# Kernel optimization log

Measured on AMD Instinct MI355X. Metric: run time of the kernel, lower is better.

Reference implementation:

```python
import jax, jax.numpy as jnp
import numpy as np

K = 1024  # attention hidden dim
H = 1024  # encoder hidden dim


def setup_inputs() -> dict:
    key = jax.random.key(0)
    ks = jax.random.split(key, 8)
    B, S = 32, 2048
    decoder_state = jax.random.normal(ks[0], (B, H), dtype=jnp.float32)
    encoder_hiddens = jax.random.normal(ks[1], (B, S, H), dtype=jnp.float32)
    # Linear params (torch convention: y = x @ W.T + b)
    Wa_w = jax.random.normal(ks[2], (1, K), dtype=jnp.float32) / np.sqrt(K)
    Wa_b = jnp.zeros((1,), dtype=jnp.float32)
    Wb_w = jax.random.normal(ks[3], (K, H), dtype=jnp.float32) / np.sqrt(H)
    Wb_b = jnp.zeros((K,), dtype=jnp.float32)
    Wc_w = jax.random.normal(ks[4], (K, H), dtype=jnp.float32) / np.sqrt(H)
    Wc_b = jnp.zeros((K,), dtype=jnp.float32)
    return {
        "decoder_state": decoder_state,
        "encoder_hiddens": encoder_hiddens,
        "Wa_w": Wa_w, "Wa_b": Wa_b,
        "Wb_w": Wb_w, "Wb_b": Wb_b,
        "Wc_w": Wc_w, "Wc_b": Wc_b,
    }


def reference(decoder_state, encoder_hiddens, Wa_w, Wa_b, Wb_w, Wb_b, Wc_w, Wc_b):
    # dec_proj: [B, K]; enc_proj: [B, S, K]
    dec_proj = decoder_state @ Wb_w.T + Wb_b
    enc_proj = jnp.einsum('bsh,kh->bsk', encoder_hiddens, Wc_w) + Wc_b
    # additive score: tanh then project to scalar -> [B, S]
    e = jnp.tanh(dec_proj[:, None, :] + enc_proj)
    scores = jnp.einsum('bsk,k->bs', e, Wa_w[0]) + Wa_b[0]
    attn = jax.nn.softmax(scores, axis=1)
    # weighted sum over sequence -> [B, H]
    context = jnp.einsum('bs,bsh->bh', attn, encoder_hiddens)
    return context
```

## Files before the change

kernel.cpp:

```cpp
#include <hip/hip_runtime.h>
#include <hip/hip_bf16.h>
#include <stdint.h>

#define B_SZ 32
#define S_SZ 2048
#define H_SZ 1024
#define K_SZ 1024
#define M_SZ (B_SZ * S_SZ)

typedef __attribute__((ext_vector_type(8))) short bf16x8;
typedef __attribute__((ext_vector_type(4))) float f32x4;


__device__ __forceinline__ short f2bf_rne(float f) {
    uint32_t u = __builtin_bit_cast(uint32_t, f);
    u += 0x7fffu + ((u >> 16) & 1u);
    return (short)(u >> 16);
}

__device__ __forceinline__ float fast_tanh(float x) {
    float ex = __expf(2.0f * x);
    return 1.0f - 2.0f / (ex + 1.0f);
}


__global__ void cvt_bf16_k(const float* __restrict__ in,
                           __hip_bfloat16* __restrict__ out, int n8) {
    int idx = blockIdx.x * blockDim.x + threadIdx.x;
    int stride = gridDim.x * blockDim.x;
    for (int i = idx; i < n8; i += stride) {
        const float4* p = (const float4*)in + (size_t)i * 2;
        float4 a = p[0], b = p[1];
        bf16x8 r;
        r[0] = f2bf_rne(a.x); r[1] = f2bf_rne(a.y);
        r[2] = f2bf_rne(a.z); r[3] = f2bf_rne(a.w);
        r[4] = f2bf_rne(b.x); r[5] = f2bf_rne(b.y);
        r[6] = f2bf_rne(b.z); r[7] = f2bf_rne(b.w);
        ((bf16x8*)out)[i] = r;
    }
}


__global__ __launch_bounds__(256) void decproj_k(
    const float* __restrict__ ds, const float* __restrict__ Wb,
    const float* __restrict__ Wb_b, const float* __restrict__ Wc_b,
    float* __restrict__ dp) {
    int g = blockIdx.x * 4 + (threadIdx.x >> 6);
    int lane = threadIdx.x & 63;
    int b = g >> 10;
    int k = g & 1023;
    const float4* wrow = (const float4*)(Wb + (size_t)k * H_SZ);
    const float4* xrow = (const float4*)(ds + (size_t)b * H_SZ);
    float sum = 0.f;
#pragma unroll
    for (int it = 0; it < 4; it++) {
        float4 w = wrow[lane + it * 64];
        float4 x = xrow[lane + it * 64];
        sum += w.x * x.x + w.y * x.y + w.z * x.z + w.w * x.w;
    }
#pragma unroll
    for (int off = 1; off < 64; off <<= 1) sum += __shfl_xor(sum, off, 64);
    if (lane == 0) dp[g] = sum + Wb_b[k] + Wc_b[k];
}


template <bool AF32>
__global__ __launch_bounds__(256) void gemm_scores_k(
    const void* __restrict__ Aptr, const __hip_bfloat16* __restrict__ Bw,
    const float* __restrict__ decp, const float* __restrict__ Wa,
    float* __restrict__ sp) {
    constexpr int ABYTES = AF32 ? 128 * 32 * 4 : 128 * 32 * 2;
    __shared__ __align__(16) unsigned char AsmRaw[ABYTES];
    __shared__ __align__(16) unsigned char BsmRaw[128 * 32 * 2];

    const int t = threadIdx.x;
    const int wave = t >> 6;
    const int lane = t & 63;
    const int wm = wave >> 1, wn = wave & 1;
    const int quad = lane >> 4;
    const int l15 = lane & 15;

    const int colBlk = blockIdx.x & 7;
    const int rowBlk = blockIdx.x >> 3;
    const int row0 = rowBlk * 128;
    const int col0 = colBlk * 128;
    const int b = row0 >> 11;

    f32x4 acc[4][4];
#pragma unroll
    for (int i = 0; i < 4; i++)
#pragma unroll
        for (int j = 0; j < 4; j++) acc[i][j] = f32x4{0.f, 0.f, 0.f, 0.f};

    const __hip_bfloat16* Ab = (const __hip_bfloat16*)Aptr;
    const float* Af = (const float*)Aptr;

    for (int k0 = 0; k0 < H_SZ; k0 += 32) {
        if constexpr (AF32) {
#pragma unroll
            for (int inst = 0; inst < 4; inst++) {
                int slot = inst * 256 + t;
                int r = slot >> 3, c4 = slot & 7;
                const float* g = Af + (size_t)(row0 + r) * H_SZ + k0 + c4 * 4;
                __builtin_amdgcn_global_load_lds(
                    (const __attribute__((address_space(1))) void*)g,
                    (__attribute__((address_space(3))) void*)(AsmRaw + inst * 4096 + wave * 1024),
                    16, 0, 0);
            }
        } else {
#pragma unroll
            for (int inst = 0; inst < 2; inst++) {
                int slot = inst * 256 + t;
                int r = slot >> 2, c8 = slot & 3;
                const __hip_bfloat16* g = Ab + (size_t)(row0 + r) * H_SZ + k0 + c8 * 8;
                __builtin_amdgcn_global_load_lds(
                    (const __attribute__((address_space(1))) void*)g,
                    (__attribute__((address_space(3))) void*)(AsmRaw + inst * 4096 + wave * 1024),
                    16, 0, 0);
            }
        }
#pragma unroll
        for (int inst = 0; inst < 2; inst++) {
            int slot = inst * 256 + t;
            int r = slot >> 2, c8 = slot & 3;
            const __hip_bfloat16* g = Bw + (size_t)(col0 + r) * H_SZ + k0 + c8 * 8;
            __builtin_amdgcn_global_load_lds(
                (const __attribute__((address_space(1))) void*)g,
                (__attribute__((address_space(3))) void*)(BsmRaw + inst * 4096 + wave * 1024),
                16, 0, 0);
        }
        __syncthreads();

        bf16x8 afr[4], bfr[4];
#pragma unroll
        for (int i = 0; i < 4; i++) {
            int r = wm * 64 + i * 16 + l15;
            if constexpr (AF32) {
                const float* ap = (const float*)AsmRaw + r * 32 + quad * 8;
                f32x4 lo = *(const f32x4*)ap;
                f32x4 hi = *(const f32x4*)(ap + 4);
                bf16x8 v;
                v[0] = f2bf_rne(lo[0]); v[1] = f2bf_rne(lo[1]);
                v[2] = f2bf_rne(lo[2]); v[3] = f2bf_rne(lo[3]);
                v[4] = f2bf_rne(hi[0]); v[5] = f2bf_rne(hi[1]);
                v[6] = f2bf_rne(hi[2]); v[7] = f2bf_rne(hi[3]);
                afr[i] = v;
            } else {
                afr[i] = *(const bf16x8*)((const __hip_bfloat16*)AsmRaw + r * 32 + quad * 8);
            }
        }
#pragma unroll
        for (int j = 0; j < 4; j++) {
            int r = wn * 64 + j * 16 + l15;
            bfr[j] = *(const bf16x8*)((const __hip_bfloat16*)BsmRaw + r * 32 + quad * 8);
        }
#pragma unroll
        for (int i = 0; i < 4; i++)
#pragma unroll
            for (int j = 0; j < 4; j++)
                acc[i][j] = __builtin_amdgcn_mfma_f32_16x16x32_bf16(afr[i], bfr[j], acc[i][j], 0, 0, 0);
        __syncthreads();
    }

    float wa_j[4], dp_j[4];
#pragma unroll
    for (int j = 0; j < 4; j++) {
        int c = col0 + wn * 64 + j * 16 + l15;
        wa_j[j] = Wa[c];
        dp_j[j] = decp[b * K_SZ + c];
    }
    const int slotIdx = colBlk * 2 + wn;
#pragma unroll
    for (int i = 0; i < 4; i++) {
#pragma unroll
        for (int r = 0; r < 4; r++) {
            float tsum = 0.f;
#pragma unroll
            for (int j = 0; j < 4; j++)
                tsum += wa_j[j] * fast_tanh(acc[i][j][r] + dp_j[j]);
#pragma unroll
            for (int off = 1; off < 16; off <<= 1) tsum += __shfl_xor(tsum, off, 64);
            if (l15 == 0) {
                int m = row0 + wm * 64 + i * 16 + quad * 4 + r;
                sp[(size_t)slotIdx * M_SZ + m] = tsum;
            }
        }
    }
}


__global__ __launch_bounds__(256) void softmax_k(
    const float* __restrict__ sp, float* __restrict__ attn) {
    int b = blockIdx.x;
    int t = threadIdx.x;
    __shared__ float wred[4];
    __shared__ float wred2[4];
    float sc[8];
    float mx = -1e30f;
#pragma unroll
    for (int u = 0; u < 8; u++) {
        int m = b * S_SZ + t + u * 256;
        float v = 0.f;
#pragma unroll
        for (int c = 0; c < 16; c++) v += sp[(size_t)c * M_SZ + m];
        sc[u] = v;
        mx = fmaxf(mx, v);
    }
#pragma unroll
    for (int off = 1; off < 64; off <<= 1) mx = fmaxf(mx, __shfl_xor(mx, off, 64));
    if ((t & 63) == 0) wred[t >> 6] = mx;
    __syncthreads();
    mx = fmaxf(fmaxf(wred[0], wred[1]), fmaxf(wred[2], wred[3]));
    float lsum = 0.f;
#pragma unroll
    for (int u = 0; u < 8; u++) { sc[u] = expf(sc[u] - mx); lsum += sc[u]; }
#pragma unroll
    for (int off = 1; off < 64; off <<= 1) lsum += __shfl_xor(lsum, off, 64);
    if ((t & 63) == 0) wred2[t >> 6] = lsum;
    __syncthreads();
    float inv = 1.f / (wred2[0] + wred2[1] + wred2[2] + wred2[3]);
#pragma unroll
    for (int u = 0; u < 8; u++) attn[b * S_SZ + t + u * 256] = sc[u] * inv;
}


__global__ __launch_bounds__(256) void ctx_part_k(
    const float* __restrict__ attn, const float* __restrict__ enc,
    float* __restrict__ cp) {
    int b = blockIdx.x >> 4;
    int c = blockIdx.x & 15;
    int t = threadIdx.x;
    __shared__ float wloc[128];
    if (t < 128) wloc[t] = attn[b * S_SZ + c * 128 + t];
    __syncthreads();
    const float4* ep = (const float4*)(enc + ((size_t)b * S_SZ + (size_t)c * 128) * H_SZ);
    float4 acc = {0.f, 0.f, 0.f, 0.f};
    for (int s = 0; s < 128; s++) {
        float w = wloc[s];
        float4 v = ep[s * 256 + t];
        acc.x += w * v.x; acc.y += w * v.y; acc.z += w * v.z; acc.w += w * v.w;
    }
    ((float4*)(cp + ((size_t)c * B_SZ + b) * H_SZ))[t] = acc;
}

__global__ void ctx_red_k(const float* __restrict__ cp, float* __restrict__ out) {
    int i = blockIdx.x * blockDim.x + threadIdx.x;
    float s = 0.f;
#pragma unroll
    for (int c = 0; c < 16; c++) s += cp[(size_t)c * (B_SZ * H_SZ) + i];
    out[i] = s;
}


extern "C" void kernel_launch(void* const* d_in, const int* in_sizes, int n_in,
                              void* d_out, int out_size, void* d_ws, size_t ws_size,
                              hipStream_t stream) {
    const float* dec  = (const float*)d_in[0];
    const float* enc  = (const float*)d_in[1];
    const float* Wa_w = (const float*)d_in[2];
    const float* Wb_w = (const float*)d_in[4];
    const float* Wb_b = (const float*)d_in[5];
    const float* Wc_w = (const float*)d_in[6];
    const float* Wc_b = (const float*)d_in[7];
    float* out = (float*)d_out;

    char* ws = (char*)d_ws;
    size_t off = 0;
    auto alloc = [&](size_t bytes) -> void* {
        void* p = ws + off;
        off += (bytes + 255) & ~(size_t)255;
        return p;
    };
    __hip_bfloat16* wc_bf = (__hip_bfloat16*)alloc((size_t)K_SZ * H_SZ * 2);
    float* dp     = (float*)alloc((size_t)B_SZ * K_SZ * 4);
    float* spart  = (float*)alloc((size_t)16 * M_SZ * 4);
    float* attn   = (float*)alloc((size_t)B_SZ * S_SZ * 4);
    float* cpart  = (float*)alloc((size_t)16 * B_SZ * H_SZ * 4);
    __hip_bfloat16* enc_bf = (__hip_bfloat16*)alloc((size_t)M_SZ * H_SZ * 2);
    const bool useBf16A = (off <= ws_size);

    cvt_bf16_k<<<512, 256, 0, stream>>>(Wc_w, wc_bf, K_SZ * H_SZ / 8);
    if (useBf16A)
        cvt_bf16_k<<<8192, 256, 0, stream>>>(enc, enc_bf, M_SZ * H_SZ / 8);
    decproj_k<<<8192, 256, 0, stream>>>(dec, Wb_w, Wb_b, Wc_b, dp);
    if (useBf16A)
        gemm_scores_k<false><<<(M_SZ / 128) * 8, 256, 0, stream>>>(enc_bf, wc_bf, dp, Wa_w, spart);
    else
        gemm_scores_k<true><<<(M_SZ / 128) * 8, 256, 0, stream>>>(enc, wc_bf, dp, Wa_w, spart);
    softmax_k<<<B_SZ, 256, 0, stream>>>(spart, attn);
    ctx_part_k<<<B_SZ * 16, 256, 0, stream>>>(attn, enc, cpart);
    ctx_red_k<<<128, 256, 0, stream>>>(cpart, out);
}
```

Measured before the change: 649.2 us.

## Read bf16 encoder copy in context pass, split sequence finer, swizzle GEMM blocks

The context-weighted-sum kernel now reads the bf16 copy of the encoder hiddens when it exists, which halves the bytes streamed in that pass. It also splits the sequence into 32 chunks of 64 instead of 16 of 128 to launch more blocks, and the reduction now sums 32 partials. The GEMM block index is remapped so that 8 consecutive blocks cover different row tiles at the same column block, aiming at better cache reuse of the weight tile. The context pass now accumulates from bf16-rounded encoder values, so results lose some precision.

```diff
diff --git a/kernel.cpp b/kernel.cpp
--- a/kernel.cpp
+++ b/kernel.cpp
@@ -16,6 +16,10 @@
     uint32_t u = __builtin_bit_cast(uint32_t, f);
     u += 0x7fffu + ((u >> 16) & 1u);
     return (short)(u >> 16);
+}
+
+__device__ __forceinline__ float bf2f(unsigned short u) {
+    return __builtin_bit_cast(float, (uint32_t)u << 16);
 }
 
 __device__ __forceinline__ float fast_tanh(float x) {
@@ -80,8 +84,9 @@
     const int quad = lane >> 4;
     const int l15 = lane & 15;
 
-    const int colBlk = blockIdx.x & 7;
-    const int rowBlk = blockIdx.x >> 3;
+    const int id = blockIdx.x;
+    const int colBlk = (id >> 3) & 7;
+    const int rowBlk = ((id >> 6) << 3) | (id & 7);
     const int row0 = rowBlk * 128;
     const int col0 = colBlk * 128;
     const int b = row0 >> 11;
@@ -224,21 +229,37 @@
 }
 
 
+template <bool BF16E>
 __global__ __launch_bounds__(256) void ctx_part_k(
-    const float* __restrict__ attn, const float* __restrict__ enc,
+    const float* __restrict__ attn, const void* __restrict__ encp,
     float* __restrict__ cp) {
-    int b = blockIdx.x >> 4;
-    int c = blockIdx.x & 15;
+    int b = blockIdx.x >> 5;
+    int c = blockIdx.x & 31;
     int t = threadIdx.x;
-    __shared__ float wloc[128];
-    if (t < 128) wloc[t] = attn[b * S_SZ + c * 128 + t];
+    __shared__ float wloc[64];
+    if (t < 64) wloc[t] = attn[b * S_SZ + c * 64 + t];
     __syncthreads();
-    const float4* ep = (const float4*)(enc + ((size_t)b * S_SZ + (size_t)c * 128) * H_SZ);
     float4 acc = {0.f, 0.f, 0.f, 0.f};
-    for (int s = 0; s < 128; s++) {
-        float w = wloc[s];
-        float4 v = ep[s * 256 + t];
-        acc.x += w * v.x; acc.y += w * v.y; acc.z += w * v.z; acc.w += w * v.w;
+    if constexpr (BF16E) {
+        const ushort4* ep = (const ushort4*)((const __hip_bfloat16*)encp +
+                              ((size_t)b * S_SZ + (size_t)c * 64) * H_SZ);
+#pragma unroll 8
+        for (int s = 0; s < 64; s++) {
+            float w = wloc[s];
+            ushort4 v = ep[s * 256 + t];
+            acc.x += w * bf2f(v.x); acc.y += w * bf2f(v.y);
+            acc.z += w * bf2f(v.z); acc.w += w * bf2f(v.w);
+        }
+    } else {
+        const float4* ep = (const float4*)((const float*)encp +
+                              ((size_t)b * S_SZ + (size_t)c * 64) * H_SZ);
+#pragma unroll 8
+        for (int s = 0; s < 64; s++) {
+            float w = wloc[s];
+            float4 v = ep[s * 256 + t];
+            acc.x += w * v.x; acc.y += w * v.y;
+            acc.z += w * v.z; acc.w += w * v.w;
+        }
     }
     ((float4*)(cp + ((size_t)c * B_SZ + b) * H_SZ))[t] = acc;
 }
@@ -247,7 +268,7 @@
     int i = blockIdx.x * blockDim.x + threadIdx.x;
     float s = 0.f;
 #pragma unroll
-    for (int c = 0; c < 16; c++) s += cp[(size_t)c * (B_SZ * H_SZ) + i];
+    for (int c = 0; c < 32; c++) s += cp[(size_t)c * (B_SZ * H_SZ) + i];
     out[i] = s;
 }
 
@@ -275,7 +296,7 @@
     float* dp     = (float*)alloc((size_t)B_SZ * K_SZ * 4);
     float* spart  = (float*)alloc((size_t)16 * M_SZ * 4);
     float* attn   = (float*)alloc((size_t)B_SZ * S_SZ * 4);
-    float* cpart  = (float*)alloc((size_t)16 * B_SZ * H_SZ * 4);
+    float* cpart  = (float*)alloc((size_t)32 * B_SZ * H_SZ * 4);
     __hip_bfloat16* enc_bf = (__hip_bfloat16*)alloc((size_t)M_SZ * H_SZ * 2);
     const bool useBf16A = (off <= ws_size);
 
@@ -288,6 +309,9 @@
     else
         gemm_scores_k<true><<<(M_SZ / 128) * 8, 256, 0, stream>>>(enc, wc_bf, dp, Wa_w, spart);
     softmax_k<<<B_SZ, 256, 0, stream>>>(spart, attn);
-    ctx_part_k<<<B_SZ * 16, 256, 0, stream>>>(attn, enc, cpart);
+    if (useBf16A)
+        ctx_part_k<true><<<B_SZ * 32, 256, 0, stream>>>(attn, enc_bf, cpart);
+    else
+        ctx_part_k<false><<<B_SZ * 32, 256, 0, stream>>>(attn, enc, cpart);
     ctx_red_k<<<128, 256, 0, stream>>>(cpart, out);
 }
```

New measurement: 613.5 us. -5.5%, faster.
